# Kernel tuning notes

Measured on AMD Instinct MI355X. Metric: run time of the kernel, lower is better.

Reference implementation:

```python
import jax, jax.numpy as jnp
import numpy as np

B, C, H, W = 8, 32, 256, 256


def setup_inputs() -> dict:
    key = jax.random.key(0)
    ks = jax.random.split(key, 9)
    x = jax.random.normal(ks[0], (B, C, H, W), dtype=jnp.float32)
    # depthwise 1x1 conv (groups=C) == per-channel scalar weight + bias
    def wb(kw, kb):
        w = jax.random.normal(kw, (C,), dtype=jnp.float32) * (1.0 / jnp.sqrt(1.0))
        b = jax.random.normal(kb, (C,), dtype=jnp.float32) * 0.1
        return w, b
    w_up, b_up = wb(ks[1], ks[2])
    w_right, b_right = wb(ks[3], ks[4])
    w_down, b_down = wb(ks[5], ks[6])
    w_left, b_left = wb(ks[7], ks[8])
    return {"x": x, "w_up": w_up, "b_up": b_up, "w_right": w_right,
            "b_right": b_right, "w_down": w_down, "b_down": b_down,
            "w_left": w_left, "b_left": b_left}


def _dir_scan(x_seq, w, b):
    """x_seq: [L, B, C, K]. h[0]=x[0]; h[t+1]=relu(w_c*h[t]+b_c+x[t+1])."""
    wb_ = w[None, :, None]
    bb_ = b[None, :, None]

    def step(h, xt):
        hn = jax.nn.relu(h * wb_ + bb_ + xt)
        return hn, hn

    _, ys = jax.lax.scan(step, x_seq[0], x_seq[1:])
    return jnp.concatenate([x_seq[:1], ys], axis=0)


def reference(x, w_up, b_up, w_right, b_right, w_down, b_down, w_left, b_left):
    xh = jnp.moveaxis(x, 2, 0)  # [H, B, C, W] for row scans
    xw = jnp.moveaxis(x, 3, 0)  # [W, B, C, H] for column scans

    top_down = jnp.moveaxis(_dir_scan(xh, w_down, b_down), 0, 2)
    top_up = jnp.moveaxis(_dir_scan(xh[::-1], w_up, b_up)[::-1], 0, 2)
    top_right = jnp.moveaxis(_dir_scan(xw, w_right, b_right), 0, 3)
    top_left = jnp.moveaxis(_dir_scan(xw[::-1], w_left, b_left)[::-1], 0, 3)

    return (top_up, top_right, top_down, top_left)
```

## Files before the change

### kernel.cpp

```cpp
#include <hip/hip_runtime.h>

#define BB 8
#define CC 32
#define HH 256
#define WW 256

__device__ __forceinline__ float step_v7(float h, float w, float b, float x) {
    float t = __fadd_rn(__fadd_rn(__fmul_rn(h, w), b), x);
    float r;
    asm volatile(
        "v_max_f32 %0, %1, 0\n\t"
        "v_min_f32 %0, %0, %2"
        : "=&v"(r)
        : "v"(t), "v"(3.3895313892515355e+38f));
    return r;
}

__global__ __launch_bounds__(256, 2) void scan_vert_v7(
    const float* __restrict__ x,
    const float* __restrict__ w_up,   const float* __restrict__ b_up,
    const float* __restrict__ w_down, const float* __restrict__ b_down,
    float* __restrict__ out_up, float* __restrict__ out_down)
{
    const int tid = blockIdx.x * 256 + threadIdx.x;
    const int w  = tid & (WW - 1);
    const int bc = tid >> 8;
    const int c  = bc & (CC - 1);
    const bool down = (blockIdx.y == 0);
    const float wc = down ? w_down[c] : w_up[c];
    const float bv = down ? b_down[c] : b_up[c];

    const long long base = (long long)bc * (HH * WW) + w;
    const long long t0   = down ? 0 : (HH - 1);
    const long long st   = down ? WW : -WW;
    const float* xs = x + base + t0 * WW;
    float*       os = (down ? out_down : out_up) + base + t0 * WW;

    float h = xs[0];
    os[0] = h;

    float buf[8];
    #pragma unroll
    for (int i = 0; i < 8; ++i) buf[i] = xs[(1 + i) * st];

    int kb = 1;
    #pragma unroll 1
    for (int g = 0; g < 30; ++g) {
        float nb[8];
        #pragma unroll
        for (int i = 0; i < 8; ++i) nb[i] = xs[(kb + 8 + i) * st];
        #pragma unroll
        for (int i = 0; i < 8; ++i) {
            h = step_v7(h, wc, bv, buf[i]);
            os[(kb + i) * st] = h;
        }
        #pragma unroll
        for (int i = 0; i < 8; ++i) buf[i] = nb[i];
        kb += 8;
    }
    float tb[7];
    #pragma unroll
    for (int i = 0; i < 7; ++i) tb[i] = xs[(249 + i) * st];
    #pragma unroll
    for (int i = 0; i < 8; ++i) {
        h = step_v7(h, wc, bv, buf[i]);
        os[(241 + i) * st] = h;
    }
    #pragma unroll
    for (int i = 0; i < 7; ++i) {
        h = step_v7(h, wc, bv, tb[i]);
        os[(249 + i) * st] = h;
    }
}

__global__ __launch_bounds__(128, 2) void scan_horiz_v7(
    const float* __restrict__ x,
    const float* __restrict__ w_right, const float* __restrict__ b_right,
    const float* __restrict__ w_left,  const float* __restrict__ b_left,
    float* __restrict__ out_right, float* __restrict__ out_left)
{
    __shared__ float tile[128 * 67];

    const int dir = blockIdx.y;
    const int tid = threadIdx.x;
    const long long R0 = (long long)blockIdx.x * 128;
    const int c = (int)((R0 >> 8) & (CC - 1));
    const float wc = dir ? w_left[c] : w_right[c];
    const float bv = dir ? b_left[c] : b_right[c];
    const float* xbase = x + R0 * WW;
    float* obase = (dir ? out_left : out_right) + R0 * WW;

    float h = 0.0f;
    for (int s = 0; s < 4; ++s) {
        const int tt = dir ? (3 - s) : s;
        const int w0 = tt * 64;

        #pragma unroll
        for (int it = 0; it < 16; ++it) {
            int idx = it * 128 + tid;
            int row = idx >> 4;
            int l   = idx & 15;
            float4 v = *(const float4*)(xbase + row * WW + w0 + l * 4);
            int a = row * 67 + l * 4;
            tile[a]     = v.x;
            tile[a + 1] = v.y;
            tile[a + 2] = v.z;
            tile[a + 3] = v.w;
        }
        __syncthreads();

        float* trow = &tile[tid * 67];
        if (dir == 0) {
            float rb[16];
            #pragma unroll
            for (int i = 0; i < 16; ++i) rb[i] = trow[i];
            #pragma unroll
            for (int q = 0; q < 4; ++q) {
                float nb[16];
                if (q < 3) {
                    #pragma unroll
                    for (int i = 0; i < 16; ++i) nb[i] = trow[16 * (q + 1) + i];
                }
                #pragma unroll
                for (int i = 0; i < 16; ++i) {
                    if (s == 0 && q == 0 && i == 0) h = rb[0];
                    else h = step_v7(h, wc, bv, rb[i]);
                    trow[16 * q + i] = h;
                }
                if (q < 3) {
                    #pragma unroll
                    for (int i = 0; i < 16; ++i) rb[i] = nb[i];
                }
            }
        } else {
            float rb[16];
            #pragma unroll
            for (int i = 0; i < 16; ++i) rb[i] = trow[48 + i];
            #pragma unroll
            for (int q = 3; q >= 0; --q) {
                float nb[16];
                if (q > 0) {
                    #pragma unroll
                    for (int i = 0; i < 16; ++i) nb[i] = trow[16 * (q - 1) + i];
                }
                #pragma unroll
                for (int i = 15; i >= 0; --i) {
                    if (s == 0 && q == 3 && i == 15) h = rb[15];
                    else h = step_v7(h, wc, bv, rb[i]);
                    trow[16 * q + i] = h;
                }
                if (q > 0) {
                    #pragma unroll
                    for (int i = 0; i < 16; ++i) rb[i] = nb[i];
                }
            }
        }
        __syncthreads();

        #pragma unroll
        for (int it = 0; it < 16; ++it) {
            int idx = it * 128 + tid;
            int row = idx >> 4;
            int l   = idx & 15;
            int a = row * 67 + l * 4;
            float4 v = make_float4(tile[a], tile[a + 1], tile[a + 2], tile[a + 3]);
            *(float4*)(obase + row * WW + w0 + l * 4) = v;
        }
        __syncthreads();
    }
}

extern "C" void kernel_launch(void* const* d_in, const int* in_sizes, int n_in,
                              void* d_out, int out_size, void* d_ws, size_t ws_size,
                              hipStream_t stream) {
    const float* x       = (const float*)d_in[0];
    const float* w_up    = (const float*)d_in[1];
    const float* b_up    = (const float*)d_in[2];
    const float* w_right = (const float*)d_in[3];
    const float* b_right = (const float*)d_in[4];
    const float* w_down  = (const float*)d_in[5];
    const float* b_down  = (const float*)d_in[6];
    const float* w_left  = (const float*)d_in[7];
    const float* b_left  = (const float*)d_in[8];

    float* out = (float*)d_out;
    const long long N = (long long)BB * CC * HH * WW;
    float* out_up    = out;
    float* out_right = out + N;
    float* out_down  = out + 2 * N;
    float* out_left  = out + 3 * N;

    scan_vert_v7<<<dim3(BB * CC, 2), 256, 0, stream>>>(
        x, w_up, b_up, w_down, b_down, out_up, out_down);

    scan_horiz_v7<<<dim3((BB * CC * HH) / 128, 2), 128, 0, stream>>>(
        x, w_right, b_right, w_left, b_left, out_right, out_left);
}
```

Measured before the change: 346.1 us.

## Fuse vertical and horizontal scans into one launch with float2 vertical lanes

Result: no change. 340.3 us (-1.7%).

```diff
diff --git a/kernel.cpp b/kernel.cpp
--- a/kernel.cpp
+++ b/kernel.cpp
@@ -5,7 +5,7 @@
 #define HH 256
 #define WW 256
 
-__device__ __forceinline__ float step_v7(float h, float w, float b, float x) {
+__device__ __forceinline__ float step_v8(float h, float w, float b, float x) {
     float t = __fadd_rn(__fadd_rn(__fmul_rn(h, w), b), x);
     float r;
     asm volatile(
@@ -16,74 +16,79 @@
     return r;
 }
 
-__global__ __launch_bounds__(256, 2) void scan_vert_v7(
+__global__ __launch_bounds__(256, 4) void irnn_fused_v8(
     const float* __restrict__ x,
-    const float* __restrict__ w_up,   const float* __restrict__ b_up,
-    const float* __restrict__ w_down, const float* __restrict__ b_down,
-    float* __restrict__ out_up, float* __restrict__ out_down)
-{
-    const int tid = blockIdx.x * 256 + threadIdx.x;
-    const int w  = tid & (WW - 1);
-    const int bc = tid >> 8;
-    const int c  = bc & (CC - 1);
-    const bool down = (blockIdx.y == 0);
-    const float wc = down ? w_down[c] : w_up[c];
-    const float bv = down ? b_down[c] : b_up[c];
-
-    const long long base = (long long)bc * (HH * WW) + w;
-    const long long t0   = down ? 0 : (HH - 1);
-    const long long st   = down ? WW : -WW;
-    const float* xs = x + base + t0 * WW;
-    float*       os = (down ? out_down : out_up) + base + t0 * WW;
-
-    float h = xs[0];
-    os[0] = h;
-
-    float buf[8];
-    #pragma unroll
-    for (int i = 0; i < 8; ++i) buf[i] = xs[(1 + i) * st];
-
-    int kb = 1;
-    #pragma unroll 1
-    for (int g = 0; g < 30; ++g) {
-        float nb[8];
-        #pragma unroll
-        for (int i = 0; i < 8; ++i) nb[i] = xs[(kb + 8 + i) * st];
-        #pragma unroll
-        for (int i = 0; i < 8; ++i) {
-            h = step_v7(h, wc, bv, buf[i]);
-            os[(kb + i) * st] = h;
-        }
-        #pragma unroll
-        for (int i = 0; i < 8; ++i) buf[i] = nb[i];
-        kb += 8;
-    }
-    float tb[7];
-    #pragma unroll
-    for (int i = 0; i < 7; ++i) tb[i] = xs[(249 + i) * st];
-    #pragma unroll
-    for (int i = 0; i < 8; ++i) {
-        h = step_v7(h, wc, bv, buf[i]);
-        os[(241 + i) * st] = h;
-    }
-    #pragma unroll
-    for (int i = 0; i < 7; ++i) {
-        h = step_v7(h, wc, bv, tb[i]);
-        os[(249 + i) * st] = h;
-    }
-}
-
-__global__ __launch_bounds__(128, 2) void scan_horiz_v7(
-    const float* __restrict__ x,
+    const float* __restrict__ w_up,    const float* __restrict__ b_up,
     const float* __restrict__ w_right, const float* __restrict__ b_right,
+    const float* __restrict__ w_down,  const float* __restrict__ b_down,
     const float* __restrict__ w_left,  const float* __restrict__ b_left,
-    float* __restrict__ out_right, float* __restrict__ out_left)
+    float* __restrict__ out_up, float* __restrict__ out_right,
+    float* __restrict__ out_down, float* __restrict__ out_left)
 {
     __shared__ float tile[128 * 67];
 
-    const int dir = blockIdx.y;
+    const int bid = blockIdx.x;
+    if (bid < BB * CC) {
+        const int bc   = bid;
+        const int c    = bc & (CC - 1);
+        const int down = (threadIdx.x < 128);
+        const int t    = threadIdx.x & 127;
+        const int w2   = t * 2;
+        const float wc = down ? w_down[c] : w_up[c];
+        const float bv = down ? b_down[c] : b_up[c];
+
+        const long long base = (long long)bc * (HH * WW) + w2;
+        const long long st   = down ? WW : -WW;
+        const long long off0 = down ? 0 : (long long)(HH - 1) * WW;
+        const float* xs = x + base + off0;
+        float*       os = (down ? out_down : out_up) + base + off0;
+
+        float2 h = *(const float2*)xs;
+        *(float2*)os = h;
+
+        float2 buf[8];
+        #pragma unroll
+        for (int i = 0; i < 8; ++i) buf[i] = *(const float2*)(xs + (1 + i) * st);
+
+        int kb = 1;
+        #pragma unroll 1
+        for (int g = 0; g < 30; ++g) {
+            float2 nb[8];
+            #pragma unroll
+            for (int i = 0; i < 8; ++i) nb[i] = *(const float2*)(xs + (kb + 8 + i) * st);
+            #pragma unroll
+            for (int i = 0; i < 8; ++i) {
+                h.x = step_v8(h.x, wc, bv, buf[i].x);
+                h.y = step_v8(h.y, wc, bv, buf[i].y);
+                *(float2*)(os + (kb + i) * st) = h;
+            }
+            #pragma unroll
+            for (int i = 0; i < 8; ++i) buf[i] = nb[i];
+            kb += 8;
+        }
+        float2 tb[7];
+        #pragma unroll
+        for (int i = 0; i < 7; ++i) tb[i] = *(const float2*)(xs + (249 + i) * st);
+        #pragma unroll
+        for (int i = 0; i < 8; ++i) {
+            h.x = step_v8(h.x, wc, bv, buf[i].x);
+            h.y = step_v8(h.y, wc, bv, buf[i].y);
+            *(float2*)(os + (241 + i) * st) = h;
+        }
+        #pragma unroll
+        for (int i = 0; i < 7; ++i) {
+            h.x = step_v8(h.x, wc, bv, tb[i].x);
+            h.y = step_v8(h.y, wc, bv, tb[i].y);
+            *(float2*)(os + (249 + i) * st) = h;
+        }
+        return;
+    }
+
+    const int hb  = bid - BB * CC;
+    const int dir = hb & 1;
+    const int rg  = hb >> 1;
     const int tid = threadIdx.x;
-    const long long R0 = (long long)blockIdx.x * 128;
+    const long long R0 = (long long)rg * 128;
     const int c = (int)((R0 >> 8) & (CC - 1));
     const float wc = dir ? w_left[c] : w_right[c];
     const float bv = dir ? b_left[c] : b_right[c];
@@ -96,8 +101,8 @@
         const int w0 = tt * 64;
 
         #pragma unroll
-        for (int it = 0; it < 16; ++it) {
-            int idx = it * 128 + tid;
+        for (int it = 0; it < 8; ++it) {
+            int idx = it * 256 + tid;
             int row = idx >> 4;
             int l   = idx & 15;
             float4 v = *(const float4*)(xbase + row * WW + w0 + l * 4);
@@ -109,57 +114,59 @@
         }
         __syncthreads();
 
-        float* trow = &tile[tid * 67];
-        if (dir == 0) {
-            float rb[16];
-            #pragma unroll
-            for (int i = 0; i < 16; ++i) rb[i] = trow[i];
-            #pragma unroll
-            for (int q = 0; q < 4; ++q) {
-                float nb[16];
-                if (q < 3) {
+        if (tid < 128) {
+            float* trow = &tile[tid * 67];
+            if (dir == 0) {
+                float rb[16];
+                #pragma unroll
+                for (int i = 0; i < 16; ++i) rb[i] = trow[i];
+                #pragma unroll
+                for (int q = 0; q < 4; ++q) {
+                    float nb[16];
+                    if (q < 3) {
+                        #pragma unroll
+                        for (int i = 0; i < 16; ++i) nb[i] = trow[16 * (q + 1) + i];
+                    }
                     #pragma unroll
-                    for (int i = 0; i < 16; ++i) nb[i] = trow[16 * (q + 1) + i];
+                    for (int i = 0; i < 16; ++i) {
+                        if (s == 0 && q == 0 && i == 0) h = rb[0];
+                        else h = step_v8(h, wc, bv, rb[i]);
+                        trow[16 * q + i] = h;
+                    }
+                    if (q < 3) {
+                        #pragma unroll
+                        for (int i = 0; i < 16; ++i) rb[i] = nb[i];
+                    }
                 }
-                #pragma unroll
-                for (int i = 0; i < 16; ++i) {
-                    if (s == 0 && q == 0 && i == 0) h = rb[0];
-                    else h = step_v7(h, wc, bv, rb[i]);
-                    trow[16 * q + i] = h;
-                }
-                if (q < 3) {
+            } else {
+                float rb[16];
+                #pragma unroll
+                for (int i = 0; i < 16; ++i) rb[i] = trow[48 + i];
+                #pragma unroll
+                for (int q = 3; q >= 0; --q) {
+                    float nb[16];
+                    if (q > 0) {
+                        #pragma unroll
+                        for (int i = 0; i < 16; ++i) nb[i] = trow[16 * (q - 1) + i];
+                    }
                     #pragma unroll
-                    for (int i = 0; i < 16; ++i) rb[i] = nb[i];
+                    for (int i = 15; i >= 0; --i) {
+                        if (s == 0 && q == 3 && i == 15) h = rb[15];
+                        else h = step_v8(h, wc, bv, rb[i]);
+                        trow[16 * q + i] = h;
+                    }
+                    if (q > 0) {
+                        #pragma unroll
+                        for (int i = 0; i < 16; ++i) rb[i] = nb[i];
+                    }
                 }
             }
-        } else {
-            float rb[16];
-            #pragma unroll
-            for (int i = 0; i < 16; ++i) rb[i] = trow[48 + i];
-            #pragma unroll
-            for (int q = 3; q >= 0; --q) {
-                float nb[16];
-                if (q > 0) {
-                    #pragma unroll
-                    for (int i = 0; i < 16; ++i) nb[i] = trow[16 * (q - 1) + i];
-                }
-                #pragma unroll
-                for (int i = 15; i >= 0; --i) {
-                    if (s == 0 && q == 3 && i == 15) h = rb[15];
-                    else h = step_v7(h, wc, bv, rb[i]);
-                    trow[16 * q + i] = h;
-                }
-                if (q > 0) {
-                    #pragma unroll
-                    for (int i = 0; i < 16; ++i) rb[i] = nb[i];
-                }
-            }
         }
         __syncthreads();
 
         #pragma unroll
-        for (int it = 0; it < 16; ++it) {
-            int idx = it * 128 + tid;
+        for (int it = 0; it < 8; ++it) {
+            int idx = it * 256 + tid;
             int row = idx >> 4;
             int l   = idx & 15;
             int a = row * 67 + l * 4;
@@ -190,9 +197,7 @@
     float* out_down  = out + 2 * N;
     float* out_left  = out + 3 * N;
 
-    scan_vert_v7<<<dim3(BB * CC, 2), 256, 0, stream>>>(
-        x, w_up, b_up, w_down, b_down, out_up, out_down);
-
-    scan_horiz_v7<<<dim3((BB * CC * HH) / 128, 2), 128, 0, stream>>>(
-        x, w_right, b_right, w_left, b_left, out_right, out_left);
+    irnn_fused_v8<<<dim3(BB * CC + 1024), 256, 0, stream>>>(
+        x, w_up, b_up, w_right, b_right, w_down, b_down, w_left, b_left,
+        out_up, out_right, out_down, out_left);
 }
```
